# Kernel tuning notes

Hardware: AMD Instinct MI355X
Metric: run time of the kernel (lower is better)

Reference implementation:

```python
import jax, jax.numpy as jnp
import numpy as np
from functools import partial

_EPS = 1e-5

def _build_R_to_F():
    R_to_F = np.zeros((9, 16), dtype=np.float32)
    F_nonzero = [
        [(0, 0, 1.0), (1, 1, 1.0), (2, 2, 1.0)], [(1, 2, 1.0), (2, 1, -1.0)],
        [(2, 0, 1.0), (0, 2, -1.0)], [(0, 1, 1.0), (1, 0, -1.0)],
        [(1, 2, 1.0), (2, 1, -1.0)], [(0, 0, 1.0), (1, 1, -1.0), (2, 2, -1.0)],
        [(0, 1, 1.0), (1, 0, 1.0)], [(0, 2, 1.0), (2, 0, 1.0)],
        [(2, 0, 1.0), (0, 2, -1.0)], [(0, 1, 1.0), (1, 0, 1.0)],
        [(0, 0, -1.0), (1, 1, 1.0), (2, 2, -1.0)], [(1, 2, 1.0), (2, 1, 1.0)],
        [(0, 1, 1.0), (1, 0, -1.0)], [(0, 2, 1.0), (2, 0, 1.0)],
        [(1, 2, 1.0), (2, 1, 1.0)], [(0, 0, -1.0), (1, 1, -1.0), (2, 2, 1.0)],
    ]
    for F_ij, nonzero in enumerate(F_nonzero):
        for R_i, R_j, sign in nonzero:
            R_to_F[R_i * 3 + R_j, F_ij] = sign
    return jnp.asarray(R_to_F)

_R_TO_F = _build_R_to_F()

def _eig_leading(F, num_iterations=50):
    # F: (..., 4, 4) symmetric. Power iteration for the MOST POSITIVE eigenvalue.
    # Shift spectrum by Frobenius norm (upper bound on spectral radius) so the
    # most positive eigenvalue is also largest in magnitude.
    shift = jnp.sqrt(jnp.sum(F * F, axis=(-2, -1), keepdims=True))  # (...,1,1)
    F_shift = F + shift * jnp.eye(4, dtype=F.dtype)
    v0 = jnp.full(F.shape[:-1], 0.5, dtype=F.dtype)  # (...,4), unit norm

    def body(_, v):
        w = jnp.einsum('...ij,...j->...i', F_shift, v)
        return w / (jnp.linalg.norm(w, axis=-1, keepdims=True) + 1e-12)

    v = jax.lax.fori_loop(0, num_iterations, body, v0)
    eig = jnp.einsum('...i,...ij,...j->...', v, F, v)  # Rayleigh quotient (unit v)
    return eig, v

def reference(X_mobile, X_target, method_iter=50):
    # X_mobile: (S, A, 3), X_target: (T, A, 3)
    num_atoms = X_mobile.shape[1]
    Xm = X_mobile - X_mobile.mean(axis=1, keepdims=True)
    Xt = X_target - X_target.mean(axis=1, keepdims=True)
    # Cross-covariance: (S, T, 3, 3)
    R = jnp.einsum('sai,taj->stij', Xm, Xt)
    S, T = R.shape[0], R.shape[1]
    F = (R.reshape(S, T, 9) @ _R_TO_F).reshape(S, T, 4, 4)
    top_eig, _ = _eig_leading(F, num_iterations=method_iter)  # (S, T)
    norms = (Xm ** 2).sum(axis=(-1, -2))[:, None] + (Xt ** 2).sum(axis=(-1, -2))[None, :]
    sqRMSD = jax.nn.relu((norms - 2.0 * top_eig) / (num_atoms + _EPS))
    return jnp.sqrt(sqRMSD)

def setup_inputs() -> dict:
    key = jax.random.key(0)
    k1, k2 = jax.random.split(key)
    X_mobile = jax.random.normal(k1, (2048, 128, 3), dtype=jnp.float32)
    X_target = jax.random.normal(k2, (2048, 128, 3), dtype=jnp.float32)
    return {"X_mobile": X_mobile, "X_target": X_target}
```

## Files before the change

kernel.cpp:

```cpp
#include <hip/hip_runtime.h>
#include <math.h>

#define NS 2048
#define NT 2048
#define NATOMS 128

typedef __attribute__((ext_vector_type(8))) short bf16x8;
typedef __attribute__((ext_vector_type(4))) float f32x4;

static __device__ __forceinline__ unsigned short f2bf(float f) {
    unsigned int u = __float_as_uint(f);
    unsigned int r = (u + 0x7fffu + ((u >> 16) & 1u)) >> 16;
    return (unsigned short)r;
}
static __device__ __forceinline__ float bf2f(unsigned short h) {
    return __uint_as_float(((unsigned int)h) << 16);
}

__global__ __launch_bounds__(64) void center_bf16_kernel(
    const float* __restrict__ X, unsigned short* __restrict__ Hi,
    unsigned short* __restrict__ Lo, float* __restrict__ norms)
{
    const int s = blockIdx.x;
    const int lane = threadIdx.x;
    const float* xs = X + (size_t)s * (NATOMS * 3);
    float x0 = xs[lane * 3 + 0];
    float y0 = xs[lane * 3 + 1];
    float z0 = xs[lane * 3 + 2];
    float x1 = xs[(lane + 64) * 3 + 0];
    float y1 = xs[(lane + 64) * 3 + 1];
    float z1 = xs[(lane + 64) * 3 + 2];
    float sx = x0 + x1, sy = y0 + y1, sz = z0 + z1;
#pragma unroll
    for (int off = 32; off > 0; off >>= 1) {
        sx += __shfl_xor(sx, off);
        sy += __shfl_xor(sy, off);
        sz += __shfl_xor(sz, off);
    }
    const float inv_n = 1.0f / (float)NATOMS;
    const float mx = sx * inv_n, my = sy * inv_n, mz = sz * inv_n;
    x0 -= mx; y0 -= my; z0 -= mz;
    x1 -= mx; y1 -= my; z1 -= mz;

    const size_t base = (size_t)s * 384;
    const float v[3][2] = {{x0, x1}, {y0, y1}, {z0, z1}};
#pragma unroll
    for (int c = 0; c < 3; ++c)
#pragma unroll
        for (int h = 0; h < 2; ++h) {
            const unsigned short hb = f2bf(v[c][h]);
            const unsigned short lb = f2bf(v[c][h] - bf2f(hb));
            Hi[base + c * 128 + h * 64 + lane] = hb;
            Lo[base + c * 128 + h * 64 + lane] = lb;
        }

    float nsq = x0 * x0 + y0 * y0 + z0 * z0 + x1 * x1 + y1 * y1 + z1 * z1;
#pragma unroll
    for (int off = 32; off > 0; off >>= 1) nsq += __shfl_xor(nsq, off);
    if (lane == 0) norms[s] = nsq;
}

__global__ __launch_bounds__(256, 7) void pair_mfma_kernel(
    const unsigned short* __restrict__ Ahi, const unsigned short* __restrict__ Alo,
    const unsigned short* __restrict__ Bhi, const unsigned short* __restrict__ Blo,
    const float* __restrict__ norm_s, const float* __restrict__ norm_t,
    float* __restrict__ out)
{
    const int tid = threadIdx.x;
    const int wave = tid >> 6;
    const int lane = tid & 63;
    const int nrow = lane & 15;
    const int kgrp = lane >> 4;
    const int sBase = blockIdx.x * 16;
    const int tBase = blockIdx.y * 64 + wave * 16;

    const size_t aOff = (size_t)(sBase + nrow) * 384 + kgrp * 8;
    const size_t bOff = (size_t)(tBase + nrow) * 384 + kgrp * 8;

    f32x4 acc[3][3];
#pragma unroll
    for (int i = 0; i < 3; ++i)
#pragma unroll
        for (int j = 0; j < 3; ++j) acc[i][j] = (f32x4){0.f, 0.f, 0.f, 0.f};

#pragma unroll
    for (int ks = 0; ks < 4; ++ks) {
        bf16x8 ah[3], al[3], bh[3], bl[3];
#pragma unroll
        for (int c = 0; c < 3; ++c) {
            ah[c] = *reinterpret_cast<const bf16x8*>(Ahi + aOff + c * 128 + ks * 32);
            al[c] = *reinterpret_cast<const bf16x8*>(Alo + aOff + c * 128 + ks * 32);
            bh[c] = *reinterpret_cast<const bf16x8*>(Bhi + bOff + c * 128 + ks * 32);
            bl[c] = *reinterpret_cast<const bf16x8*>(Blo + bOff + c * 128 + ks * 32);
        }
#pragma unroll
        for (int i = 0; i < 3; ++i)
#pragma unroll
            for (int j = 0; j < 3; ++j)
                acc[i][j] = __builtin_amdgcn_mfma_f32_16x16x32_bf16(
                    ah[i], bh[j], acc[i][j], 0, 0, 0);
#pragma unroll
        for (int i = 0; i < 3; ++i)
#pragma unroll
            for (int j = 0; j < 3; ++j)
                acc[i][j] = __builtin_amdgcn_mfma_f32_16x16x32_bf16(
                    ah[i], bl[j], acc[i][j], 0, 0, 0);
#pragma unroll
        for (int i = 0; i < 3; ++i)
#pragma unroll
            for (int j = 0; j < 3; ++j)
                acc[i][j] = __builtin_amdgcn_mfma_f32_16x16x32_bf16(
                    al[i], bh[j], acc[i][j], 0, 0, 0);
    }

    float D0[4], D1[4], D2[4], D3[4];
    float E01[4], E02[4], E03[4], E12[4], E13[4], E23[4];
    float FRO[4];
    float q0[4], q1[4], q2[4], q3[4];
#pragma unroll
    for (int u = 0; u < 4; ++u) {
        const float Sxx = acc[0][0][u], Sxy = acc[0][1][u], Sxz = acc[0][2][u];
        const float Syx = acc[1][0][u], Syy = acc[1][1][u], Syz = acc[1][2][u];
        const float Szx = acc[2][0][u], Szy = acc[2][1][u], Szz = acc[2][2][u];
        const float F00 =  Sxx + Syy + Szz;
        const float F11 =  Sxx - Syy - Szz;
        const float F22 = -Sxx + Syy - Szz;
        const float F33 = -Sxx - Syy + Szz;
        const float F01 = Syz - Szy;
        const float F02 = Szx - Sxz;
        const float F03 = Sxy - Syx;
        const float F12 = Sxy + Syx;
        const float F13 = Sxz + Szx;
        const float F23 = Syz + Szy;
        const float fro = sqrtf(F00 * F00 + F11 * F11 + F22 * F22 + F33 * F33 +
                                2.0f * (F01 * F01 + F02 * F02 + F03 * F03 +
                                        F12 * F12 + F13 * F13 + F23 * F23));
        FRO[u] = fro;
        D0[u] = F00 + fro;
        D1[u] = F11 + fro;
        D2[u] = F22 + fro;
        D3[u] = F33 + fro;
        E01[u] = F01; E02[u] = F02; E03[u] = F03;
        E12[u] = F12; E13[u] = F13; E23[u] = F23;
        q0[u] = 0.5f; q1[u] = 0.5f; q2[u] = 0.5f; q3[u] = 0.5f;
    }

    for (int blk = 0; blk < 10; ++blk) {
#pragma unroll
        for (int k = 0; k < 5; ++k) {
#pragma unroll
            for (int u = 0; u < 4; ++u) {
                const float w0 = fmaf(E03[u], q3[u], fmaf(E02[u], q2[u],
                                 fmaf(E01[u], q1[u], D0[u] * q0[u])));
                const float w1 = fmaf(E13[u], q3[u], fmaf(E12[u], q2[u],
                                 fmaf(D1[u], q1[u], E01[u] * q0[u])));
                const float w2 = fmaf(E23[u], q3[u], fmaf(D2[u], q2[u],
                                 fmaf(E12[u], q1[u], E02[u] * q0[u])));
                const float w3 = fmaf(D3[u], q3[u], fmaf(E23[u], q2[u],
                                 fmaf(E13[u], q1[u], E03[u] * q0[u])));
                q0[u] = w0; q1[u] = w1; q2[u] = w2; q3[u] = w3;
            }
        }
#pragma unroll
        for (int u = 0; u < 4; ++u) {
            const float a0 = q0[u], a1 = q1[u], a2 = q2[u], a3 = q3[u];
            const float nn = a0 * a0 + a1 * a1 + a2 * a2 + a3 * a3;
            const float sc = __builtin_amdgcn_rsqf(nn);
            q0[u] = a0 * sc; q1[u] = a1 * sc;
            q2[u] = a2 * sc; q3[u] = a3 * sc;
        }
    }

    const float inv_na = 1.0f / (128.0f + 1e-5f);
    const float Gb = norm_t[tBase + nrow];
#pragma unroll
    for (int u = 0; u < 4; ++u) {
        const int srow = sBase + kgrp * 4 + u;
        const float Ga = norm_s[srow];
        const float a0 = q0[u], a1 = q1[u], a2 = q2[u], a3 = q3[u];
        const float m0 = D0[u] * a0 + E01[u] * a1 + E02[u] * a2 + E03[u] * a3;
        const float m1 = E01[u] * a0 + D1[u] * a1 + E12[u] * a2 + E13[u] * a3;
        const float m2 = E02[u] * a0 + E12[u] * a1 + D2[u] * a2 + E23[u] * a3;
        const float m3 = E03[u] * a0 + E13[u] * a1 + E23[u] * a2 + D3[u] * a3;
        const float num = a0 * m0 + a1 * m1 + a2 * m2 + a3 * m3;
        const float den = a0 * a0 + a1 * a1 + a2 * a2 + a3 * a3;
        const float eig = num * __builtin_amdgcn_rcpf(den) - FRO[u];
        float sq = (Ga + Gb - 2.0f * eig) * inv_na;
        out[(size_t)srow * NT + tBase + nrow] = sqrtf(fmaxf(sq, 0.0f));
    }
}

extern "C" void kernel_launch(void* const* d_in, const int* in_sizes, int n_in,
                              void* d_out, int out_size, void* d_ws, size_t ws_size,
                              hipStream_t stream) {
    const float* Xm = (const float*)d_in[0];
    const float* Xt = (const float*)d_in[1];
    float* out = (float*)d_out;

    unsigned short* ws16 = (unsigned short*)d_ws;
    unsigned short* Ahi = ws16;
    unsigned short* Alo = Ahi + (size_t)NS * 384;
    unsigned short* Bhi = Alo + (size_t)NS * 384;
    unsigned short* Blo = Bhi + (size_t)NT * 384;
    float* norm_m = (float*)(Blo + (size_t)NT * 384);
    float* norm_t = norm_m + NS;

    center_bf16_kernel<<<NS, 64, 0, stream>>>(Xm, Ahi, Alo, norm_m);
    center_bf16_kernel<<<NT, 64, 0, stream>>>(Xt, Bhi, Blo, norm_t);

    dim3 grid(NS / 16, NT / 64);
    pair_mfma_kernel<<<grid, 256, 0, stream>>>(Ahi, Alo, Bhi, Blo,
                                               norm_m, norm_t, out);
}
```

Before: 139.5 us.

## Cut register pressure in pair MFMA kernel via staged loads and recomputed shift

Stops fully unrolling the K loop and splits each step into three stages: hi*hi, then hi*lo, then lo*hi with Bhi reloaded. Sched barriers and an asm barrier keep the stages apart so fewer bf16 fragments are live at once. The per-element Frobenius shift is no longer stored; it is recomputed from the trace of the shifted diagonal, and offsets become 32-bit. The aim is to lower VGPR usage and relax launch bounds from 7 to 6 blocks, at the cost of redundant Bhi loads, less scheduling freedom and a slightly different rounding of the shift.

```diff
diff --git a/kernel.cpp b/kernel.cpp
--- a/kernel.cpp
+++ b/kernel.cpp
@@ -60,7 +60,7 @@
     if (lane == 0) norms[s] = nsq;
 }
 
-__global__ __launch_bounds__(256, 7) void pair_mfma_kernel(
+__global__ __launch_bounds__(256, 6) void pair_mfma_kernel(
     const unsigned short* __restrict__ Ahi, const unsigned short* __restrict__ Alo,
     const unsigned short* __restrict__ Bhi, const unsigned short* __restrict__ Blo,
     const float* __restrict__ norm_s, const float* __restrict__ norm_t,
@@ -74,8 +74,8 @@
     const int sBase = blockIdx.x * 16;
     const int tBase = blockIdx.y * 64 + wave * 16;
 
-    const size_t aOff = (size_t)(sBase + nrow) * 384 + kgrp * 8;
-    const size_t bOff = (size_t)(tBase + nrow) * 384 + kgrp * 8;
+    const unsigned aOff = (unsigned)((sBase + nrow) * 384 + kgrp * 8);
+    const unsigned bOff = (unsigned)((tBase + nrow) * 384 + kgrp * 8);
 
     f32x4 acc[3][3];
 #pragma unroll
@@ -83,39 +83,57 @@
 #pragma unroll
         for (int j = 0; j < 3; ++j) acc[i][j] = (f32x4){0.f, 0.f, 0.f, 0.f};
 
-#pragma unroll
+#pragma unroll 1
     for (int ks = 0; ks < 4; ++ks) {
-        bf16x8 ah[3], al[3], bh[3], bl[3];
-#pragma unroll
-        for (int c = 0; c < 3; ++c) {
-            ah[c] = *reinterpret_cast<const bf16x8*>(Ahi + aOff + c * 128 + ks * 32);
-            al[c] = *reinterpret_cast<const bf16x8*>(Alo + aOff + c * 128 + ks * 32);
-            bh[c] = *reinterpret_cast<const bf16x8*>(Bhi + bOff + c * 128 + ks * 32);
-            bl[c] = *reinterpret_cast<const bf16x8*>(Blo + bOff + c * 128 + ks * 32);
-        }
-#pragma unroll
-        for (int i = 0; i < 3; ++i)
-#pragma unroll
-            for (int j = 0; j < 3; ++j)
-                acc[i][j] = __builtin_amdgcn_mfma_f32_16x16x32_bf16(
-                    ah[i], bh[j], acc[i][j], 0, 0, 0);
-#pragma unroll
-        for (int i = 0; i < 3; ++i)
-#pragma unroll
-            for (int j = 0; j < 3; ++j)
-                acc[i][j] = __builtin_amdgcn_mfma_f32_16x16x32_bf16(
-                    ah[i], bl[j], acc[i][j], 0, 0, 0);
-#pragma unroll
-        for (int i = 0; i < 3; ++i)
-#pragma unroll
-            for (int j = 0; j < 3; ++j)
-                acc[i][j] = __builtin_amdgcn_mfma_f32_16x16x32_bf16(
-                    al[i], bh[j], acc[i][j], 0, 0, 0);
+        const unsigned ak = aOff + ks * 32;
+        const unsigned bk = bOff + ks * 32;
+        {
+            bf16x8 ah[3], bh[3];
+#pragma unroll
+            for (int c = 0; c < 3; ++c) {
+                ah[c] = *reinterpret_cast<const bf16x8*>(Ahi + ak + c * 128);
+                bh[c] = *reinterpret_cast<const bf16x8*>(Bhi + bk + c * 128);
+            }
+#pragma unroll
+            for (int i = 0; i < 3; ++i)
+#pragma unroll
+                for (int j = 0; j < 3; ++j)
+                    acc[i][j] = __builtin_amdgcn_mfma_f32_16x16x32_bf16(
+                        ah[i], bh[j], acc[i][j], 0, 0, 0);
+            __builtin_amdgcn_sched_barrier(0);
+            bf16x8 bl[3];
+#pragma unroll
+            for (int c = 0; c < 3; ++c)
+                bl[c] = *reinterpret_cast<const bf16x8*>(Blo + bk + c * 128);
+#pragma unroll
+            for (int i = 0; i < 3; ++i)
+#pragma unroll
+                for (int j = 0; j < 3; ++j)
+                    acc[i][j] = __builtin_amdgcn_mfma_f32_16x16x32_bf16(
+                        ah[i], bl[j], acc[i][j], 0, 0, 0);
+            __builtin_amdgcn_sched_barrier(0);
+        }
+        {
+            bf16x8 al[3], bh2[3];
+            unsigned bkL = bk;
+            asm volatile("" : "+v"(bkL));
+#pragma unroll
+            for (int c = 0; c < 3; ++c) {
+                al[c]  = *reinterpret_cast<const bf16x8*>(Alo + ak + c * 128);
+                bh2[c] = *reinterpret_cast<const bf16x8*>(Bhi + bkL + c * 128);
+            }
+#pragma unroll
+            for (int i = 0; i < 3; ++i)
+#pragma unroll
+                for (int j = 0; j < 3; ++j)
+                    acc[i][j] = __builtin_amdgcn_mfma_f32_16x16x32_bf16(
+                        al[i], bh2[j], acc[i][j], 0, 0, 0);
+            __builtin_amdgcn_sched_barrier(0);
+        }
     }
 
     float D0[4], D1[4], D2[4], D3[4];
     float E01[4], E02[4], E03[4], E12[4], E13[4], E23[4];
-    float FRO[4];
     float q0[4], q1[4], q2[4], q3[4];
 #pragma unroll
     for (int u = 0; u < 4; ++u) {
@@ -135,7 +153,6 @@
         const float fro = sqrtf(F00 * F00 + F11 * F11 + F22 * F22 + F33 * F33 +
                                 2.0f * (F01 * F01 + F02 * F02 + F03 * F03 +
                                         F12 * F12 + F13 * F13 + F23 * F23));
-        FRO[u] = fro;
         D0[u] = F00 + fro;
         D1[u] = F11 + fro;
         D2[u] = F22 + fro;
@@ -178,13 +195,14 @@
         const int srow = sBase + kgrp * 4 + u;
         const float Ga = norm_s[srow];
         const float a0 = q0[u], a1 = q1[u], a2 = q2[u], a3 = q3[u];
+        const float fro = (((D0[u] + D1[u]) + D2[u]) + D3[u]) * 0.25f;
         const float m0 = D0[u] * a0 + E01[u] * a1 + E02[u] * a2 + E03[u] * a3;
         const float m1 = E01[u] * a0 + D1[u] * a1 + E12[u] * a2 + E13[u] * a3;
         const float m2 = E02[u] * a0 + E12[u] * a1 + D2[u] * a2 + E23[u] * a3;
         const float m3 = E03[u] * a0 + E13[u] * a1 + E23[u] * a2 + D3[u] * a3;
         const float num = a0 * m0 + a1 * m1 + a2 * m2 + a3 * m3;
         const float den = a0 * a0 + a1 * a1 + a2 * a2 + a3 * a3;
-        const float eig = num * __builtin_amdgcn_rcpf(den) - FRO[u];
+        const float eig = num * __builtin_amdgcn_rcpf(den) - fro;
         float sq = (Ga + Gb - 2.0f * eig) * inv_na;
         out[(size_t)srow * NT + tBase + nrow] = sqrtf(fmaxf(sq, 0.0f));
     }
```

After: 146.5 us. 5.0% more time.
